# Optimization experiments

Measured on AMD Instinct MI355X. Metric: run time of the kernel, lower is better.

Reference implementation:

```python
import jax, jax.numpy as jnp
import numpy as np

CONF_THRESH = 0.01
TOP_K = 200
NMS_THRESH = 0.45


def setup_inputs() -> dict:
    key = jax.random.key(0)
    k1, k2, k3, k4, k5 = jax.random.split(key, 5)
    B, N, C = 32, 8732, 21
    return {
        "loc_data": jax.random.normal(k1, (B, N, 4), jnp.float32),
        "conf_data": jax.random.normal(k2, (B, N, C), jnp.float32),
        "pose_data": jax.random.normal(k3, (B, N, 32), jnp.float32),
        "line_data": jax.random.normal(k4, (B, N, 3), jnp.float32),
        "dbox_list": jax.random.uniform(k5, (N, 4), jnp.float32),
    }


def decode(loc, dbox):
    # loc, dbox: [N,4]; variances 0.1 / 0.2 as in the torch decode()
    cxcy = dbox[:, :2] + loc[:, :2] * 0.1 * dbox[:, 2:]
    wh = dbox[:, 2:] * jnp.exp(loc[:, 2:] * 0.2)
    mins = cxcy - wh / 2.0
    maxs = mins + wh
    return jnp.concatenate([mins, maxs], axis=1)  # [N,4] xyxy


def nms_class(boxes, scores, poses, lines):
    """Greedy NMS for one (batch, class). boxes [N,4], scores [N] (softmax probs).
    Matches torch nm_suppression: candidates are the top_k by score above
    conf_thresh; suppress IoU > overlap; at most top_k kept."""
    s0 = jnp.where(scores > CONF_THRESH, scores, -jnp.inf)
    _, cand_idx = jax.lax.top_k(s0, TOP_K)  # descending-score candidate pool
    cb = boxes[cand_idx]                     # [K,4]
    cs = s0[cand_idx]                        # [K], -inf where below threshold
    x1, y1, x2, y2 = cb[:, 0], cb[:, 1], cb[:, 2], cb[:, 3]
    area = (x2 - x1) * (y2 - y1)
    K = TOP_K
    ar = jnp.arange(K)

    def step(s, _):
        i = jnp.argmax(s)
        take = jnp.isfinite(s[i])
        xx1 = jnp.maximum(x1, x1[i])
        yy1 = jnp.maximum(y1, y1[i])
        xx2 = jnp.minimum(x2, x2[i])
        yy2 = jnp.minimum(y2, y2[i])
        inter = jnp.clip(xx2 - xx1, 0.0) * jnp.clip(yy2 - yy1, 0.0)
        union = area - inter + area[i]
        iou = inter / union
        supp = (iou > NMS_THRESH) | (ar == i)
        s_new = jnp.where(take & supp, -jnp.inf, s)
        return s_new, (i, take)

    _, (pos, take) = jax.lax.scan(step, cs, None, length=K)
    gi = cand_idx[pos]  # global box indices of kept detections [K]
    row = jnp.concatenate(
        [scores[gi][:, None], boxes[gi], poses[gi], lines[gi]], axis=1
    )  # [K, 1+4+32+3] = [200, 40]
    return row * take[:, None].astype(row.dtype)


def reference(loc_data, conf_data, pose_data, line_data, dbox_list):
    conf = jax.nn.softmax(conf_data, axis=-1)                       # [B,N,C]
    boxes = jax.vmap(decode, in_axes=(0, None))(loc_data, dbox_list)  # [B,N,4]
    per_cls = jax.vmap(nms_class, in_axes=(None, 1, None, None))    # over classes
    per_batch = jax.vmap(per_cls, in_axes=(0, 0, 0, 0))             # over batch
    out = per_batch(boxes, conf, pose_data, line_data)              # [B,C,200,40]
    return out.at[:, 0].set(0.0)  # class 0 (background) is skipped in torch loop
```

## Files before the change

kernel.cpp:

```cpp
#include <hip/hip_runtime.h>
#include <math.h>

#define BB 32
#define NN 8732
#define CC 21
#define TOPK 200
#define NPOSE 32
#define NLINE 3
#define NBINS 2048
#define CAP 1024
#define ROWW 40

__device__ __forceinline__ double fexp(double x) {
  const double LOG2E = 1.4426950408889634074;
  const double LN2HI = 6.93147180369123816490e-01;
  const double LN2LO = 1.90821492927058770002e-10;
  double kd = rint(x * LOG2E);
  double r = fma(-kd, LN2HI, x);
  r = fma(-kd, LN2LO, r);
  double p = 2.08767569878680989792e-09;
  p = fma(p, r, 2.50521083854417187751e-08);
  p = fma(p, r, 2.75573192239858906526e-07);
  p = fma(p, r, 2.75573192239858925110e-06);
  p = fma(p, r, 2.48015873015873015873e-05);
  p = fma(p, r, 1.98412698412698412698e-04);
  p = fma(p, r, 1.38888888888888888889e-03);
  p = fma(p, r, 8.33333333333333333333e-03);
  p = fma(p, r, 4.16666666666666666667e-02);
  p = fma(p, r, 1.66666666666666666667e-01);
  p = fma(p, r, 0.5);
  p = fma(p, r, 1.0);
  p = fma(p, r, 1.0);
  int k = (int)kd;
  k = k < -1020 ? -1020 : (k > 1020 ? 1020 : k);
  double sc = __longlong_as_double((long long)(1023 + k) << 52);
  return p * sc;
}

__global__ __launch_bounds__(256) void score_kernel(
    const float* __restrict__ conf, float* __restrict__ scores) {
  __shared__ __align__(16) float buf[256 * CC];
  const int tid = threadIdx.x;
  const int i0 = blockIdx.x * 256;
  const int base = i0 * CC;
  int total = BB * NN * CC - base;
  if (total > 256 * CC) total = 256 * CC;
  {
    const float4* g4 = (const float4*)(conf + base);
    float4* b4 = (float4*)buf;
    const int n4 = total >> 2;
    for (int t = tid; t < n4; t += 256) b4[t] = g4[t];
  }
  __syncthreads();
  const int i = i0 + tid;
  if (i >= BB * NN) return;
  float* p = buf + tid * CC;
  float m = p[0];
#pragma unroll
  for (int c = 1; c < CC; ++c) m = fmaxf(m, p[c]);
#pragma unroll 1
  for (int c = 0; c < CC; ++c) p[c] = (float)fexp((double)(p[c] - m));
  float r0 = p[0] + p[8], r1 = p[1] + p[9], r2 = p[2] + p[10], r3 = p[3] + p[11];
  float r4 = p[4] + p[12], r5 = p[5] + p[13], r6 = p[6] + p[14], r7 = p[7] + p[15];
  float sum = ((r0 + r1) + (r2 + r3)) + ((r4 + r5) + (r6 + r7));
  sum += p[16]; sum += p[17]; sum += p[18]; sum += p[19]; sum += p[20];
  const int b = i / NN, n = i - b * NN;
#pragma unroll 1
  for (int c = 0; c < CC; ++c)
    scores[((size_t)b * CC + c) * NN + n] = p[c] / sum;
}

__global__ __launch_bounds__(256) void aux_kernel(
    const float* __restrict__ conf, float2* __restrict__ aux) {
  int i = blockIdx.x * 256 + threadIdx.x;
  if (i >= BB * NN) return;
  const float* p = conf + (size_t)i * CC;
  float m = p[0];
#pragma unroll
  for (int c = 1; c < CC; ++c) m = fmaxf(m, p[c]);
  float e[CC];
#pragma unroll 1
  for (int c = 0; c < CC; ++c) e[c] = (float)fexp((double)(p[c] - m));
  float r0 = e[0] + e[8], r1 = e[1] + e[9], r2 = e[2] + e[10], r3 = e[3] + e[11];
  float r4 = e[4] + e[12], r5 = e[5] + e[13], r6 = e[6] + e[14], r7 = e[7] + e[15];
  float sum = ((r0 + r1) + (r2 + r3)) + ((r4 + r5) + (r6 + r7));
  sum += e[16]; sum += e[17]; sum += e[18]; sum += e[19]; sum += e[20];
  aux[i] = make_float2(m, sum);
}

__device__ __forceinline__ int score_bin(float s) {
  unsigned u = __float_as_uint(s);
  int bin = (int)(u >> 15) - 30720;
  return bin < 0 ? 0 : (bin > NBINS - 1 ? NBINS - 1 : bin);
}

__global__ __launch_bounds__(256) void nms_kernel(
    const float* __restrict__ loc, const float* __restrict__ conf,
    const float* __restrict__ pose, const float* __restrict__ line,
    const float* __restrict__ dbox, const float* __restrict__ scores,
    const float2* __restrict__ aux, int mode, float* __restrict__ out) {
  const int bc = blockIdx.x;
  const int b = bc / CC, c = bc - b * CC;
  const int tid = threadIdx.x;
  float* outSlab = out + (size_t)bc * (TOPK * ROWW);

  {
    float4 z = make_float4(0.f, 0.f, 0.f, 0.f);
    float4* o4 = (float4*)outSlab;
    for (int i = tid; i < TOPK * ROWW / 4; i += 256) o4[i] = z;
  }
  if (c == 0) return;

  __shared__ int hist[NBINS];
  __shared__ int chunkSum[256];
  __shared__ float cscore[CAP];
  __shared__ int cidx[CAP];
  __shared__ float bx1[TOPK], by1[TOPK], bx2[TOPK], by2[TOPK], barea[TOPK];
  __shared__ int kept[TOPK];
  __shared__ int sBT, sCnt, sKept;

  for (int i = tid; i < NBINS; i += 256) hist[i] = 0;
  if (tid == 0) sCnt = 0;
  __syncthreads();

  const float* scoresB = scores + ((size_t)b * CC + c) * NN;
  const float2* auxB = aux + (size_t)b * NN;
  const float* confB = conf + (size_t)b * NN * CC + c;

  if (mode == 2) {
    float4 v[9];
#pragma unroll
    for (int k = 0; k < 8; ++k)
      v[k] = *(const float4*)(scoresB + k * 1024 + tid * 4);
    if (tid < 135)
      v[8] = *(const float4*)(scoresB + 8192 + tid * 4);
    else
      v[8] = make_float4(-1.f, -1.f, -1.f, -1.f);

#pragma unroll
    for (int k = 0; k < 9; ++k) {
      float s0 = v[k].x, s1 = v[k].y, s2 = v[k].z, s3 = v[k].w;
      if (s0 > 0.01f) atomicAdd(&hist[score_bin(s0)], 1);
      if (s1 > 0.01f) atomicAdd(&hist[score_bin(s1)], 1);
      if (s2 > 0.01f) atomicAdd(&hist[score_bin(s2)], 1);
      if (s3 > 0.01f) atomicAdd(&hist[score_bin(s3)], 1);
    }
    __syncthreads();

    {
      int s8 = 0;
#pragma unroll
      for (int k = 0; k < 8; ++k) s8 += hist[tid * 8 + k];
      chunkSum[tid] = s8;
    }
    __syncthreads();
    if (tid == 0) {
      int cum = 0, bt = 0;
      for (int ch = 255; ch >= 0; --ch) {
        if (cum + chunkSum[ch] >= TOPK) {
          for (int bin = ch * 8 + 7;; --bin) {
            cum += hist[bin];
            if (cum >= TOPK || bin == ch * 8) { bt = bin; break; }
          }
          break;
        }
        cum += chunkSum[ch];
      }
      sBT = bt;
    }
    __syncthreads();
    const int bt = sBT;

#pragma unroll
    for (int k = 0; k < 9; ++k) {
      float sv[4] = {v[k].x, v[k].y, v[k].z, v[k].w};
#pragma unroll
      for (int j = 0; j < 4; ++j) {
        float s = sv[j];
        if (s > 0.01f && score_bin(s) >= bt) {
          int p = atomicAdd(&sCnt, 1);
          if (p < CAP) { cscore[p] = s; cidx[p] = k * 1024 + tid * 4 + j; }
        }
      }
    }
  } else {
    for (int n = tid; n < NN; n += 256) {
      float s;
      if (mode == 1) {
        float2 a = auxB[n];
        s = (float)fexp((double)(confB[(size_t)n * CC] - a.x)) / a.y;
      } else {
        const float* p = conf + ((size_t)b * NN + n) * CC;
        float mm = p[0];
        for (int c2 = 1; c2 < CC; ++c2) mm = fmaxf(mm, p[c2]);
        float e[CC];
        for (int c2 = 0; c2 < CC; ++c2) e[c2] = (float)fexp((double)(p[c2] - mm));
        float r0 = e[0] + e[8], r1 = e[1] + e[9], r2 = e[2] + e[10], r3 = e[3] + e[11];
        float r4 = e[4] + e[12], r5 = e[5] + e[13], r6 = e[6] + e[14], r7 = e[7] + e[15];
        float sum = ((r0 + r1) + (r2 + r3)) + ((r4 + r5) + (r6 + r7));
        sum += e[16]; sum += e[17]; sum += e[18]; sum += e[19]; sum += e[20];
        s = e[c] / sum;
      }
      if (s > 0.01f) atomicAdd(&hist[score_bin(s)], 1);
    }
    __syncthreads();
    {
      int s8 = 0;
#pragma unroll
      for (int k = 0; k < 8; ++k) s8 += hist[tid * 8 + k];
      chunkSum[tid] = s8;
    }
    __syncthreads();
    if (tid == 0) {
      int cum = 0, bt = 0;
      for (int ch = 255; ch >= 0; --ch) {
        if (cum + chunkSum[ch] >= TOPK) {
          for (int bin = ch * 8 + 7;; --bin) {
            cum += hist[bin];
            if (cum >= TOPK || bin == ch * 8) { bt = bin; break; }
          }
          break;
        }
        cum += chunkSum[ch];
      }
      sBT = bt;
    }
    __syncthreads();
    const int bt = sBT;
    for (int n = tid; n < NN; n += 256) {
      float s;
      if (mode == 1) {
        float2 a = auxB[n];
        s = (float)fexp((double)(confB[(size_t)n * CC] - a.x)) / a.y;
      } else {
        const float* p = conf + ((size_t)b * NN + n) * CC;
        float mm = p[0];
        for (int c2 = 1; c2 < CC; ++c2) mm = fmaxf(mm, p[c2]);
        float e[CC];
        for (int c2 = 0; c2 < CC; ++c2) e[c2] = (float)fexp((double)(p[c2] - mm));
        float r0 = e[0] + e[8], r1 = e[1] + e[9], r2 = e[2] + e[10], r3 = e[3] + e[11];
        float r4 = e[4] + e[12], r5 = e[5] + e[13], r6 = e[6] + e[14], r7 = e[7] + e[15];
        float sum = ((r0 + r1) + (r2 + r3)) + ((r4 + r5) + (r6 + r7));
        sum += e[16]; sum += e[17]; sum += e[18]; sum += e[19]; sum += e[20];
        s = e[c] / sum;
      }
      if (s > 0.01f && score_bin(s) >= bt) {
        int p = atomicAdd(&sCnt, 1);
        if (p < CAP) { cscore[p] = s; cidx[p] = n; }
      }
    }
  }
  __syncthreads();
  const int M = sCnt < CAP ? sCnt : CAP;
  if (M == 0) return;

  int P = 1;
  while (P < M) P <<= 1;
  for (int i = M + tid; i < P; i += 256) {
    cscore[i] = -1e30f;
    cidx[i] = 0x7fffffff;
  }
  __syncthreads();
  for (int k = 2; k <= P; k <<= 1) {
    for (int j = k >> 1; j > 0; j >>= 1) {
      for (int i = tid; i < P; i += 256) {
        int ixj = i ^ j;
        if (ixj > i) {
          float si = cscore[i], sj = cscore[ixj];
          int ii = cidx[i], ij = cidx[ixj];
          bool agt = (si > sj) || (si == sj && ii < ij);
          bool up = ((i & k) == 0);
          if (up ? !agt : agt) {
            cscore[i] = sj; cscore[ixj] = si;
            cidx[i] = ij;  cidx[ixj] = ii;
          }
        }
      }
      __syncthreads();
    }
  }

  const int K = M < TOPK ? M : TOPK;

  const float* locB = loc + (size_t)b * NN * 4;
  for (int t = tid; t < K; t += 256) {
    int n = cidx[t];
    float l0 = locB[(size_t)n * 4 + 0], l1 = locB[(size_t)n * 4 + 1];
    float l2 = locB[(size_t)n * 4 + 2], l3 = locB[(size_t)n * 4 + 3];
    float d0 = dbox[(size_t)n * 4 + 0], d1 = dbox[(size_t)n * 4 + 1];
    float d2 = dbox[(size_t)n * 4 + 2], d3 = dbox[(size_t)n * 4 + 3];
    float cx = d0 + (l0 * 0.1f) * d2;
    float cy = d1 + (l1 * 0.1f) * d3;
    float w = d2 * (float)fexp((double)(l2 * 0.2f));
    float h = d3 * (float)fexp((double)(l3 * 0.2f));
    float x1 = cx - w * 0.5f;
    float y1 = cy - h * 0.5f;
    float x2 = x1 + w;
    float y2 = y1 + h;
    bx1[t] = x1; by1[t] = y1; bx2[t] = x2; by2[t] = y2;
    barea[t] = (x2 - x1) * (y2 - y1);
  }
  __syncthreads();

  if (tid < 64) {
    const int lane = tid;
    float X1[4], Y1[4], X2[4], Y2[4], AR[4];
    unsigned aliveBits = 0;
#pragma unroll
    for (int s = 0; s < 4; ++s) {
      int l = s * 64 + lane;
      if (l < K) {
        X1[s] = bx1[l]; Y1[s] = by1[l]; X2[s] = bx2[l]; Y2[s] = by2[l];
        AR[s] = barea[l];
        aliveBits |= 1u << s;
      } else {
        X1[s] = 0.f; Y1[s] = 0.f; X2[s] = 0.f; Y2[s] = 0.f; AR[s] = 0.f;
      }
    }
#pragma unroll
    for (int s = 0; s < 4; ++s) {
      int jmax = K - s * 64;
      if (jmax > 64) jmax = 64;
      for (int jj = 0; jj < jmax; ++jj) {
        unsigned abits = (unsigned)__shfl((int)aliveBits, jj, 64);
        if (!((abits >> s) & 1)) continue;
        const int j = s * 64 + jj;
        float x1j = __shfl(X1[s], jj, 64);
        float y1j = __shfl(Y1[s], jj, 64);
        float x2j = __shfl(X2[s], jj, 64);
        float y2j = __shfl(Y2[s], jj, 64);
        float aj  = __shfl(AR[s], jj, 64);
#pragma unroll
        for (int t2 = 0; t2 < 4; ++t2) {
          int l = t2 * 64 + lane;
          if (((aliveBits >> t2) & 1) && l > j) {
            float xx1 = fmaxf(X1[t2], x1j);
            float yy1 = fmaxf(Y1[t2], y1j);
            float xx2 = fminf(X2[t2], x2j);
            float yy2 = fminf(Y2[t2], y2j);
            float iw = fmaxf(xx2 - xx1, 0.0f);
            float ih = fmaxf(yy2 - yy1, 0.0f);
            float inter = iw * ih;
            float uni = (AR[t2] - inter) + aj;
            if (inter / uni > 0.45f) aliveBits &= ~(1u << t2);
          }
        }
      }
    }
    int base2 = 0;
#pragma unroll
    for (int s = 0; s < 4; ++s) {
      unsigned long long mb = __ballot((int)((aliveBits >> s) & 1));
      if ((aliveBits >> s) & 1) {
        int rank = base2 + __popcll(mb & ((1ull << lane) - 1));
        kept[rank] = s * 64 + lane;
      }
      base2 += __popcll(mb);
    }
    if (lane == 0) sKept = base2;
  }
  __syncthreads();

  const int nk = sKept;
  const float* poseB = pose + (size_t)b * NN * NPOSE;
  const float* lineB = line + (size_t)b * NN * NLINE;
  for (int t = tid; t < nk; t += 256) {
    int j = kept[t];
    int n = cidx[j];
    float* row = outSlab + (size_t)t * ROWW;
    row[0] = cscore[j];
    row[1] = bx1[j];
    row[2] = by1[j];
    row[3] = bx2[j];
    row[4] = by2[j];
    const float4* p4 = (const float4*)(poseB + (size_t)n * NPOSE);
#pragma unroll
    for (int q = 0; q < 8; ++q) {
      float4 pv = p4[q];
      row[5 + 4 * q + 0] = pv.x;
      row[5 + 4 * q + 1] = pv.y;
      row[5 + 4 * q + 2] = pv.z;
      row[5 + 4 * q + 3] = pv.w;
    }
    row[37] = lineB[(size_t)n * NLINE + 0];
    row[38] = lineB[(size_t)n * NLINE + 1];
    row[39] = lineB[(size_t)n * NLINE + 2];
  }
}

extern "C" void kernel_launch(void* const* d_in, const int* in_sizes, int n_in,
                              void* d_out, int out_size, void* d_ws, size_t ws_size,
                              hipStream_t stream) {
  const float* loc  = (const float*)d_in[0];
  const float* conf = (const float*)d_in[1];
  const float* pose = (const float*)d_in[2];
  const float* line = (const float*)d_in[3];
  const float* dbox = (const float*)d_in[4];
  float* out = (float*)d_out;

  const size_t scoreBytes = (size_t)BB * CC * NN * sizeof(float);
  const size_t auxBytes   = (size_t)BB * NN * sizeof(float2);

  int mode;
  float* scores = nullptr;
  float2* aux = nullptr;
  if (ws_size >= scoreBytes) {
    mode = 2; scores = (float*)d_ws;
  } else if (ws_size >= auxBytes) {
    mode = 1; aux = (float2*)d_ws;
  } else {
    mode = 0;
  }

  const int total = BB * NN;
  if (mode == 2) {
    score_kernel<<<(total + 255) / 256, 256, 0, stream>>>(conf, scores);
  } else if (mode == 1) {
    aux_kernel<<<(total + 255) / 256, 256, 0, stream>>>(conf, aux);
  }
  nms_kernel<<<BB * CC, 256, 0, stream>>>(loc, conf, pose, line, dbox,
                                          scores, aux, mode, out);
}
```

Baseline: 192.0 us.

## Parallelize NMS via suppression bitmask matrix and wave-parallel threshold scan

Replaces the single-wave serial greedy NMS with an all-waves computation of a pairwise IoU suppression bitmask, followed by one thread doing a bitmask sweep. The histogram threshold search now uses a wave prefix scan instead of a serial loop over chunk sums on one thread. Output zeroing is restricted to rows past the kept count rather than zeroing the whole slab first, and the softmax in score_kernel keeps values in registers with full unrolling. The bitmask approach computes all K² IoUs without early skipping and adds shared memory for the mask, while the final sweep remains serial.

After: 187.1 us. 1.03x faster.

```diff
diff --git a/kernel.cpp b/kernel.cpp
--- a/kernel.cpp
+++ b/kernel.cpp
@@ -37,7 +37,7 @@
   return p * sc;
 }
 
-__global__ __launch_bounds__(256) void score_kernel(
+__global__ __launch_bounds__(256, 4) void score_kernel(
     const float* __restrict__ conf, float* __restrict__ scores) {
   __shared__ __align__(16) float buf[256 * CC];
   const int tid = threadIdx.x;
@@ -54,20 +54,24 @@
   __syncthreads();
   const int i = i0 + tid;
   if (i >= BB * NN) return;
-  float* p = buf + tid * CC;
-  float m = p[0];
-#pragma unroll
-  for (int c = 1; c < CC; ++c) m = fmaxf(m, p[c]);
-#pragma unroll 1
-  for (int c = 0; c < CC; ++c) p[c] = (float)fexp((double)(p[c] - m));
-  float r0 = p[0] + p[8], r1 = p[1] + p[9], r2 = p[2] + p[10], r3 = p[3] + p[11];
-  float r4 = p[4] + p[12], r5 = p[5] + p[13], r6 = p[6] + p[14], r7 = p[7] + p[15];
+  const float* p = buf + tid * CC;
+  float x[CC];
+#pragma unroll
+  for (int c = 0; c < CC; ++c) x[c] = p[c];
+  float m = x[0];
+#pragma unroll
+  for (int c = 1; c < CC; ++c) m = fmaxf(m, x[c]);
+  float e[CC];
+#pragma unroll
+  for (int c = 0; c < CC; ++c) e[c] = (float)fexp((double)(x[c] - m));
+  float r0 = e[0] + e[8], r1 = e[1] + e[9], r2 = e[2] + e[10], r3 = e[3] + e[11];
+  float r4 = e[4] + e[12], r5 = e[5] + e[13], r6 = e[6] + e[14], r7 = e[7] + e[15];
   float sum = ((r0 + r1) + (r2 + r3)) + ((r4 + r5) + (r6 + r7));
-  sum += p[16]; sum += p[17]; sum += p[18]; sum += p[19]; sum += p[20];
+  sum += e[16]; sum += e[17]; sum += e[18]; sum += e[19]; sum += e[20];
   const int b = i / NN, n = i - b * NN;
-#pragma unroll 1
+#pragma unroll
   for (int c = 0; c < CC; ++c)
-    scores[((size_t)b * CC + c) * NN + n] = p[c] / sum;
+    scores[((size_t)b * CC + c) * NN + n] = e[c] / sum;
 }
 
 __global__ __launch_bounds__(256) void aux_kernel(
@@ -94,6 +98,25 @@
   return bin < 0 ? 0 : (bin > NBINS - 1 ? NBINS - 1 : bin);
 }
 
+__device__ __forceinline__ float score_at(int mode, int b, int c, int n,
+                                          const float* conf, const float2* auxB,
+                                          const float* confB) {
+  if (mode == 1) {
+    float2 a = auxB[n];
+    return (float)fexp((double)(confB[(size_t)n * CC] - a.x)) / a.y;
+  }
+  const float* p = conf + ((size_t)b * NN + n) * CC;
+  float mm = p[0];
+  for (int c2 = 1; c2 < CC; ++c2) mm = fmaxf(mm, p[c2]);
+  float e[CC];
+  for (int c2 = 0; c2 < CC; ++c2) e[c2] = (float)fexp((double)(p[c2] - mm));
+  float r0 = e[0] + e[8], r1 = e[1] + e[9], r2 = e[2] + e[10], r3 = e[3] + e[11];
+  float r4 = e[4] + e[12], r5 = e[5] + e[13], r6 = e[6] + e[14], r7 = e[7] + e[15];
+  float sum = ((r0 + r1) + (r2 + r3)) + ((r4 + r5) + (r6 + r7));
+  sum += e[16]; sum += e[17]; sum += e[18]; sum += e[19]; sum += e[20];
+  return e[c] / sum;
+}
+
 __global__ __launch_bounds__(256) void nms_kernel(
     const float* __restrict__ loc, const float* __restrict__ conf,
     const float* __restrict__ pose, const float* __restrict__ line,
@@ -102,33 +125,35 @@
   const int bc = blockIdx.x;
   const int b = bc / CC, c = bc - b * CC;
   const int tid = threadIdx.x;
+  const int wv = tid >> 6, lane = tid & 63;
   float* outSlab = out + (size_t)bc * (TOPK * ROWW);
-
-  {
-    float4 z = make_float4(0.f, 0.f, 0.f, 0.f);
+  const float4 z4 = make_float4(0.f, 0.f, 0.f, 0.f);
+
+  if (c == 0) {
     float4* o4 = (float4*)outSlab;
-    for (int i = tid; i < TOPK * ROWW / 4; i += 256) o4[i] = z;
-  }
-  if (c == 0) return;
+    for (int i = tid; i < TOPK * ROWW / 4; i += 256) o4[i] = z4;
+    return;
+  }
 
   __shared__ int hist[NBINS];
-  __shared__ int chunkSum[256];
   __shared__ float cscore[CAP];
   __shared__ int cidx[CAP];
   __shared__ float bx1[TOPK], by1[TOPK], bx2[TOPK], by2[TOPK], barea[TOPK];
+  __shared__ unsigned long long supp[TOPK * 4];
   __shared__ int kept[TOPK];
+  __shared__ int waveTot[4];
   __shared__ int sBT, sCnt, sKept;
 
   for (int i = tid; i < NBINS; i += 256) hist[i] = 0;
-  if (tid == 0) sCnt = 0;
+  if (tid == 0) { sCnt = 0; sBT = 0; }
   __syncthreads();
 
   const float* scoresB = scores + ((size_t)b * CC + c) * NN;
   const float2* auxB = aux + (size_t)b * NN;
   const float* confB = conf + (size_t)b * NN * CC + c;
 
+  float4 v[9];
   if (mode == 2) {
-    float4 v[9];
 #pragma unroll
     for (int k = 0; k < 8; ++k)
       v[k] = *(const float4*)(scoresB + k * 1024 + tid * 4);
@@ -136,41 +161,50 @@
       v[8] = *(const float4*)(scoresB + 8192 + tid * 4);
     else
       v[8] = make_float4(-1.f, -1.f, -1.f, -1.f);
-
 #pragma unroll
     for (int k = 0; k < 9; ++k) {
-      float s0 = v[k].x, s1 = v[k].y, s2 = v[k].z, s3 = v[k].w;
-      if (s0 > 0.01f) atomicAdd(&hist[score_bin(s0)], 1);
-      if (s1 > 0.01f) atomicAdd(&hist[score_bin(s1)], 1);
-      if (s2 > 0.01f) atomicAdd(&hist[score_bin(s2)], 1);
-      if (s3 > 0.01f) atomicAdd(&hist[score_bin(s3)], 1);
-    }
-    __syncthreads();
-
-    {
-      int s8 = 0;
-#pragma unroll
-      for (int k = 0; k < 8; ++k) s8 += hist[tid * 8 + k];
-      chunkSum[tid] = s8;
-    }
-    __syncthreads();
-    if (tid == 0) {
-      int cum = 0, bt = 0;
-      for (int ch = 255; ch >= 0; --ch) {
-        if (cum + chunkSum[ch] >= TOPK) {
-          for (int bin = ch * 8 + 7;; --bin) {
-            cum += hist[bin];
-            if (cum >= TOPK || bin == ch * 8) { bt = bin; break; }
-          }
-          break;
-        }
-        cum += chunkSum[ch];
+      if (v[k].x > 0.01f) atomicAdd(&hist[score_bin(v[k].x)], 1);
+      if (v[k].y > 0.01f) atomicAdd(&hist[score_bin(v[k].y)], 1);
+      if (v[k].z > 0.01f) atomicAdd(&hist[score_bin(v[k].z)], 1);
+      if (v[k].w > 0.01f) atomicAdd(&hist[score_bin(v[k].w)], 1);
+    }
+  } else {
+    for (int n = tid; n < NN; n += 256) {
+      float s = score_at(mode, b, c, n, conf, auxB, confB);
+      if (s > 0.01f) atomicAdd(&hist[score_bin(s)], 1);
+    }
+  }
+  __syncthreads();
+
+  int s8 = 0;
+#pragma unroll
+  for (int k = 0; k < 8; ++k) s8 += hist[tid * 8 + k];
+  int cs = s8;
+#pragma unroll
+  for (int d = 1; d < 64; d <<= 1) {
+    int t = __shfl_down(cs, d, 64);
+    if (lane + d < 64) cs += t;
+  }
+  if (lane == 0) waveTot[wv] = cs;
+  __syncthreads();
+  {
+    int higher = 0;
+    for (int g = wv + 1; g < 4; ++g) higher += waveTot[g];
+    int incl = cs + higher;
+    int excl = incl - s8;
+    if (excl < TOPK && incl >= TOPK) {
+      int cum = excl, bt = tid * 8;
+      for (int bin = tid * 8 + 7;; --bin) {
+        cum += hist[bin];
+        if (cum >= TOPK || bin == tid * 8) { bt = bin; break; }
       }
       sBT = bt;
     }
-    __syncthreads();
-    const int bt = sBT;
-
+  }
+  __syncthreads();
+  const int bt = sBT;
+
+  if (mode == 2) {
 #pragma unroll
     for (int k = 0; k < 9; ++k) {
       float sv[4] = {v[k].x, v[k].y, v[k].z, v[k].w};
@@ -185,65 +219,7 @@
     }
   } else {
     for (int n = tid; n < NN; n += 256) {
-      float s;
-      if (mode == 1) {
-        float2 a = auxB[n];
-        s = (float)fexp((double)(confB[(size_t)n * CC] - a.x)) / a.y;
-      } else {
-        const float* p = conf + ((size_t)b * NN + n) * CC;
-        float mm = p[0];
-        for (int c2 = 1; c2 < CC; ++c2) mm = fmaxf(mm, p[c2]);
-        float e[CC];
-        for (int c2 = 0; c2 < CC; ++c2) e[c2] = (float)fexp((double)(p[c2] - mm));
-        float r0 = e[0] + e[8], r1 = e[1] + e[9], r2 = e[2] + e[10], r3 = e[3] + e[11];
-        float r4 = e[4] + e[12], r5 = e[5] + e[13], r6 = e[6] + e[14], r7 = e[7] + e[15];
-        float sum = ((r0 + r1) + (r2 + r3)) + ((r4 + r5) + (r6 + r7));
-        sum += e[16]; sum += e[17]; sum += e[18]; sum += e[19]; sum += e[20];
-        s = e[c] / sum;
-      }
-      if (s > 0.01f) atomicAdd(&hist[score_bin(s)], 1);
-    }
-    __syncthreads();
-    {
-      int s8 = 0;
-#pragma unroll
-      for (int k = 0; k < 8; ++k) s8 += hist[tid * 8 + k];
-      chunkSum[tid] = s8;
-    }
-    __syncthreads();
-    if (tid == 0) {
-      int cum = 0, bt = 0;
-      for (int ch = 255; ch >= 0; --ch) {
-        if (cum + chunkSum[ch] >= TOPK) {
-          for (int bin = ch * 8 + 7;; --bin) {
-            cum += hist[bin];
-            if (cum >= TOPK || bin == ch * 8) { bt = bin; break; }
-          }
-          break;
-        }
-        cum += chunkSum[ch];
-      }
-      sBT = bt;
-    }
-    __syncthreads();
-    const int bt = sBT;
-    for (int n = tid; n < NN; n += 256) {
-      float s;
-      if (mode == 1) {
-        float2 a = auxB[n];
-        s = (float)fexp((double)(confB[(size_t)n * CC] - a.x)) / a.y;
-      } else {
-        const float* p = conf + ((size_t)b * NN + n) * CC;
-        float mm = p[0];
-        for (int c2 = 1; c2 < CC; ++c2) mm = fmaxf(mm, p[c2]);
-        float e[CC];
-        for (int c2 = 0; c2 < CC; ++c2) e[c2] = (float)fexp((double)(p[c2] - mm));
-        float r0 = e[0] + e[8], r1 = e[1] + e[9], r2 = e[2] + e[10], r3 = e[3] + e[11];
-        float r4 = e[4] + e[12], r5 = e[5] + e[13], r6 = e[6] + e[14], r7 = e[7] + e[15];
-        float sum = ((r0 + r1) + (r2 + r3)) + ((r4 + r5) + (r6 + r7));
-        sum += e[16]; sum += e[17]; sum += e[18]; sum += e[19]; sum += e[20];
-        s = e[c] / sum;
-      }
+      float s = score_at(mode, b, c, n, conf, auxB, confB);
       if (s > 0.01f && score_bin(s) >= bt) {
         int p = atomicAdd(&sCnt, 1);
         if (p < CAP) { cscore[p] = s; cidx[p] = n; }
@@ -252,7 +228,11 @@
   }
   __syncthreads();
   const int M = sCnt < CAP ? sCnt : CAP;
-  if (M == 0) return;
+  if (M == 0) {
+    float4* o4 = (float4*)outSlab;
+    for (int i = tid; i < TOPK * ROWW / 4; i += 256) o4[i] = z4;
+    return;
+  }
 
   int P = 1;
   while (P < M) P <<= 1;
@@ -302,62 +282,55 @@
   }
   __syncthreads();
 
-  if (tid < 64) {
-    const int lane = tid;
-    float X1[4], Y1[4], X2[4], Y2[4], AR[4];
-    unsigned aliveBits = 0;
-#pragma unroll
-    for (int s = 0; s < 4; ++s) {
-      int l = s * 64 + lane;
-      if (l < K) {
-        X1[s] = bx1[l]; Y1[s] = by1[l]; X2[s] = bx2[l]; Y2[s] = by2[l];
-        AR[s] = barea[l];
-        aliveBits |= 1u << s;
-      } else {
-        X1[s] = 0.f; Y1[s] = 0.f; X2[s] = 0.f; Y2[s] = 0.f; AR[s] = 0.f;
-      }
-    }
-#pragma unroll
-    for (int s = 0; s < 4; ++s) {
-      int jmax = K - s * 64;
-      if (jmax > 64) jmax = 64;
-      for (int jj = 0; jj < jmax; ++jj) {
-        unsigned abits = (unsigned)__shfl((int)aliveBits, jj, 64);
-        if (!((abits >> s) & 1)) continue;
-        const int j = s * 64 + jj;
-        float x1j = __shfl(X1[s], jj, 64);
-        float y1j = __shfl(Y1[s], jj, 64);
-        float x2j = __shfl(X2[s], jj, 64);
-        float y2j = __shfl(Y2[s], jj, 64);
-        float aj  = __shfl(AR[s], jj, 64);
-#pragma unroll
-        for (int t2 = 0; t2 < 4; ++t2) {
-          int l = t2 * 64 + lane;
-          if (((aliveBits >> t2) & 1) && l > j) {
-            float xx1 = fmaxf(X1[t2], x1j);
-            float yy1 = fmaxf(Y1[t2], y1j);
-            float xx2 = fminf(X2[t2], x2j);
-            float yy2 = fminf(Y2[t2], y2j);
-            float iw = fmaxf(xx2 - xx1, 0.0f);
-            float ih = fmaxf(yy2 - yy1, 0.0f);
-            float inter = iw * ih;
-            float uni = (AR[t2] - inter) + aj;
-            if (inter / uni > 0.45f) aliveBits &= ~(1u << t2);
-          }
-        }
-      }
-    }
-    int base2 = 0;
-#pragma unroll
-    for (int s = 0; s < 4; ++s) {
-      unsigned long long mb = __ballot((int)((aliveBits >> s) & 1));
-      if ((aliveBits >> s) & 1) {
-        int rank = base2 + __popcll(mb & ((1ull << lane) - 1));
-        kept[rank] = s * 64 + lane;
-      }
-      base2 += __popcll(mb);
-    }
-    if (lane == 0) sKept = base2;
+  {
+    const int l = wv * 64 + lane;
+    float lx1 = 0.f, ly1 = 0.f, lx2 = 0.f, ly2 = 0.f, lar = 0.f;
+    const bool lvalid = l < K;
+    if (lvalid) { lx1 = bx1[l]; ly1 = by1[l]; lx2 = bx2[l]; ly2 = by2[l]; lar = barea[l]; }
+    const int wtop = wv * 64 + 63;
+    for (int j = 0; j < K; ++j) {
+      unsigned long long mres = 0;
+      if (wtop > j) {
+        float jx1 = bx1[j], jy1 = by1[j], jx2 = bx2[j], jy2 = by2[j], ja = barea[j];
+        float xx1 = fmaxf(lx1, jx1);
+        float yy1 = fmaxf(ly1, jy1);
+        float xx2 = fminf(lx2, jx2);
+        float yy2 = fminf(ly2, jy2);
+        float iw = fmaxf(xx2 - xx1, 0.0f);
+        float ih = fmaxf(yy2 - yy1, 0.0f);
+        float inter = iw * ih;
+        float uni = (lar - inter) + ja;
+        bool hit = lvalid & (l > j) & (inter / uni > 0.45f);
+        mres = __ballot((int)hit);
+      }
+      if (lane == 0) supp[j * 4 + wv] = mres;
+    }
+  }
+  __syncthreads();
+
+  if (tid == 0) {
+    unsigned long long alive[4];
+#pragma unroll
+    for (int w = 0; w < 4; ++w) {
+      int cnt = K - w * 64;
+      alive[w] = cnt <= 0 ? 0ull : (cnt >= 64 ? ~0ull : ((1ull << cnt) - 1ull));
+    }
+    int nk = 0;
+#pragma unroll
+    for (int w = 0; w < 4; ++w) {
+      while (alive[w]) {
+        int bit = __ffsll(alive[w]) - 1;
+        int j = w * 64 + bit;
+        kept[nk++] = j;
+        unsigned long long r0 = supp[j * 4 + 0];
+        unsigned long long r1 = supp[j * 4 + 1];
+        unsigned long long r2 = supp[j * 4 + 2];
+        unsigned long long r3 = supp[j * 4 + 3];
+        alive[w] &= ~(1ull << bit);
+        alive[0] &= ~r0; alive[1] &= ~r1; alive[2] &= ~r2; alive[3] &= ~r3;
+      }
+    }
+    sKept = nk;
   }
   __syncthreads();
 
@@ -386,6 +359,11 @@
     row[38] = lineB[(size_t)n * NLINE + 1];
     row[39] = lineB[(size_t)n * NLINE + 2];
   }
+  {
+    const int zq = (TOPK - nk) * 10;
+    float4* o4 = (float4*)(outSlab + (size_t)nk * ROWW);
+    for (int q = tid; q < zq; q += 256) o4[q] = z4;
+  }
 }
 
 extern "C" void kernel_launch(void* const* d_in, const int* in_sizes, int n_in,
```
